# Performance work log

Measured on AMD Instinct MI355X. Metric: run time of the kernel, lower is better.

The kernel has to match this reference:

```python
import jax, jax.numpy as jnp
import numpy as np

B, L, C, H, W = 8, 8, 64, 56, 56
K = 3
EPS = 1e-5


def setup_inputs() -> dict:
    key = jax.random.key(0)
    ks = jax.random.split(key, 7)
    s = lambda k, shape, sc=0.05: jax.random.normal(k, shape, dtype=jnp.float32) * sc
    return {
        "x": jax.random.normal(ks[0], (B, L, C, H, W), dtype=jnp.float32),
        "temporal_w": s(ks[1], (C, C)),        # Conv3d 1x1x1 C->C
        "temporal_b": s(ks[2], (C,)),
        "fc_w": s(ks[3], (C,)),                # Conv3d 1x1x1 C->1
        "fc_b": s(ks[4], (1,)),
        "conv_w": s(ks[5], (C, C, K, K), 0.1), # self.weight [1,1,Co,Ci,k,k] core
        "conv_b": s(ks[6], (C,)),              # self.bias [1,1,Co] core
        "bn_gamma": jnp.ones((C,), jnp.float32),
        "bn_beta": jnp.zeros((C,), jnp.float32),
    }


def reference(x, temporal_w, temporal_b, fc_w, fc_b, conv_w, conv_b, bn_gamma, bn_beta):
    b, l, c, h, w = x.shape
    # ---- generateweight_fourier ----
    xin = jnp.transpose(x, (0, 2, 1, 3, 4))                # [B,C,L,H,W]
    f = jnp.fft.fft2(xin, axes=(3, 4), norm='ortho')       # spatial FFT
    f = jnp.fft.fft(f, axis=2, norm='ortho')               # temporal FFT
    allxin = xin + 0.01 * jnp.abs(f) * xin                 # Fourier2 attention + residual
    pooled = allxin.mean(axis=(3, 4))                      # AdaptiveAvgPool3d((None,1,1)) -> [B,C,L]
    # temporalconv: 1x1x1 Conv3d C->C on [B,C,L,1,1]
    calib = jnp.einsum('oc,bcl->bol', temporal_w, pooled) + temporal_b[None, :, None]  # [B,C,L]
    # fc: 1x1x1 Conv3d C->1
    fcout = jnp.einsum('c,bcl->bl', fc_w, pooled) + fc_b[0]                            # [B,L]
    # finalweight: weight[1,1,Co,Ci,k,k] * (calib+1) broadcast over Ci -> [B,L,Co,Ci,k,k]
    calib_blc = jnp.transpose(calib, (0, 2, 1)) + 1.0      # [B,L,Ci]
    fw = conv_w[None, None] * calib_blc[:, :, None, :, None, None]
    fb = conv_b[None, None, :] * (fcout + 1.0)[:, :, None] # [B,L,Co]
    # ---- dynamic per-(sample,frame) conv2d (groups = b*l) ----
    x_flat = x.reshape(b * l, c, h, w)
    fw_flat = fw.reshape(b * l, c, c, K, K)
    fb_flat = fb.reshape(b * l, c)

    def per_sample(xi, wi):
        return jax.lax.conv_general_dilated(
            xi[None], wi, window_strides=(1, 1), padding=[(1, 1), (1, 1)],
            dimension_numbers=('NCHW', 'OIHW', 'NCHW'))[0]

    out = jax.vmap(per_sample)(x_flat, fw_flat) + fb_flat[:, :, None, None]
    out = x_flat + out                                     # residual (gate=False)
    # BatchNorm2d (training-mode batch statistics)
    mean = out.mean(axis=(0, 2, 3), keepdims=True)
    var = out.var(axis=(0, 2, 3), keepdims=True)
    out = (out - mean) * jax.lax.rsqrt(var + EPS)
    out = out * bn_gamma[None, :, None, None] + bn_beta[None, :, None, None]
    out = out * jax.nn.sigmoid(out)                        # SiLU
    return out.reshape(b, l, c, h, w)
```

## Files before the change

### kernel.cpp

```cpp
#include <hip/hip_runtime.h>
#include <cmath>

#define HW 3136
#define NF 64
#define NBLK2 448
#define YROWS 29
#define YPX 1624

typedef __attribute__((ext_vector_type(8))) short short8;
typedef __attribute__((ext_vector_type(4))) float float4a;

__device__ __forceinline__ unsigned short f2bf(float f) {
    unsigned int u = __float_as_uint(f);
    u += 0x7fffu + ((u >> 16) & 1u);
    return (unsigned short)(u >> 16);
}
__device__ __forceinline__ float bf2f(unsigned short u) {
    return __uint_as_float(((unsigned int)u) << 16);
}

__global__ __launch_bounds__(256)
void pack_kernel(const float* __restrict__ cw,
                 unsigned short* __restrict__ Ffix,
                 unsigned short* __restrict__ Wp,
                 unsigned short* __restrict__ Fs1) {
    if (blockIdx.x < 64) {
        int idx = blockIdx.x * 256 + threadIdx.x;
        int j    = idx & 7;
        int lane = (idx >> 3) & 63;
        int ks   = (idx >> 9) & 3;
        int t    = (idx >> 11) & 3;
        int p    = (idx >> 13) & 1;
        int mn = t * 16 + (lane & 15);
        int k  = ks * 32 + (lane >> 4) * 8 + j;
        float val = 0.f;
        if (mn < 56 && k < 112) {
            int h = k >> 1;
            int prod = (mn * h) % 56;
            float ang = -6.2831853071795864f * (float)prod / 56.0f;
            float cr = cosf(ang);
            float ci = sinf(ang);
            if (p == 0) val = (k & 1) ? -ci : cr;
            else        val = (k & 1) ?  cr : ci;
        }
        Ffix[idx] = f2bf(val);
    } else if (blockIdx.x < 208) {
        int idx = (blockIdx.x - 64) * 256 + threadIdx.x;
        if (idx < 36864) {
            int i  = idx & 63;
            int o  = (idx >> 6) & 63;
            int kk = idx >> 12;
            Wp[idx] = f2bf(cw[(o * 64 + i) * 9 + kk]);
        }
    } else {
        int idx = (blockIdx.x - 208) * 256 + threadIdx.x;
        int j  = idx & 7;
        int ln = (idx >> 3) & 63;
        int ks = (idx >> 9) & 1;
        int mt = (idx >> 10) & 3;
        int m = mt * 16 + (ln & 15);
        int k = ks * 32 + (ln >> 4) * 8 + j;
        float val = 0.f;
        if (k < 56) {
            if (m < 29) {
                int prod = (m * k) % 56;
                val = cosf(-6.2831853071795864f * (float)prod / 56.0f);
            } else if (m >= 32 && m < 61) {
                int mm = m - 32;
                int prod = (mm * k) % 56;
                val = sinf(-6.2831853071795864f * (float)prod / 56.0f);
            }
        }
        Fs1[idx] = f2bf(val);
    }
}

__global__ __launch_bounds__(256)
void dft2d_kernel(const float* __restrict__ x,
                  const unsigned short* __restrict__ Fs1,
                  const unsigned short* __restrict__ Ffix,
                  unsigned short* __restrict__ Y) {
    const int bid = blockIdx.x;
    const int l  = bid & 7;
    const int bc = bid >> 3;
    const int c  = bc & 63;
    const int b  = bc >> 6;
    const int tid  = threadIdx.x;
    const int lane = tid & 63;
    const int wv   = tid >> 6;
    const int n    = lane & 15;
    const int q    = lane >> 4;

    __shared__ unsigned short xT[64 * 68];
    __shared__ unsigned short P[32 * 136];

    for (int t = tid; t < 656; t += 256) {
        if (t < 384) ((unsigned int*)xT)[(t / 6) * 34 + 28 + (t % 6)] = 0u;
        else         ((unsigned int*)xT)[56 * 34 + (t - 384)] = 0u;
    }
    const float* xp = x + ((size_t)((b * 8 + l) * 64 + c)) * HW;
    for (int t = tid; t < 784; t += 256) {
        int h = t / 14, w4 = t - h * 14;
        float4 v = *(const float4*)(xp + h * 56 + w4 * 4);
        xT[(w4 * 4 + 0) * 68 + h] = f2bf(v.x);
        xT[(w4 * 4 + 1) * 68 + h] = f2bf(v.y);
        xT[(w4 * 4 + 2) * 68 + h] = f2bf(v.z);
        xT[(w4 * 4 + 3) * 68 + h] = f2bf(v.w);
    }
    __syncthreads();

    {
        float4a acc[4];
        #pragma unroll
        for (int nt = 0; nt < 4; ++nt) acc[nt] = (float4a){0.f, 0.f, 0.f, 0.f};
        #pragma unroll
        for (int ks = 0; ks < 2; ++ks) {
            short8 afr = *(const short8*)(Fs1 + ((size_t)((wv * 2 + ks) * 64 + lane)) * 8);
            #pragma unroll
            for (int nt = 0; nt < 4; ++nt) {
                short8 bfr = *(const short8*)(xT + (nt * 16 + n) * 68 + ks * 32 + q * 8);
                acc[nt] = __builtin_amdgcn_mfma_f32_16x16x32_bf16(afr, bfr, acc[nt], 0, 0, 0);
            }
        }
        #pragma unroll
        for (int nt = 0; nt < 4; ++nt)
            #pragma unroll
            for (int r = 0; r < 4; ++r) {
                int m = wv * 16 + q * 4 + r;
                P[(m & 31) * 136 + 2 * (nt * 16 + n) + (m >> 5)] = f2bf(acc[nt][r]);
            }
    }
    __syncthreads();

    {
        const int p  = wv >> 1;
        const int ch = wv & 1;
        short8 afr[2][4];
        #pragma unroll
        for (int mt = 0; mt < 2; ++mt)
            #pragma unroll
            for (int ks = 0; ks < 4; ++ks)
                afr[mt][ks] = *(const short8*)(P + (mt * 16 + n) * 136 + ks * 32 + q * 8);
        float4a acc[2][2];
        #pragma unroll
        for (int mt = 0; mt < 2; ++mt)
            #pragma unroll
            for (int u = 0; u < 2; ++u) acc[mt][u] = (float4a){0.f, 0.f, 0.f, 0.f};
        #pragma unroll
        for (int ks = 0; ks < 4; ++ks)
            #pragma unroll
            for (int u = 0; u < 2; ++u) {
                int nt = ch * 2 + u;
                short8 bfr = *(const short8*)(Ffix + ((size_t)(((p * 4 + nt) * 4 + ks) * 64 + lane)) * 8);
                #pragma unroll
                for (int mt = 0; mt < 2; ++mt)
                    acc[mt][u] = __builtin_amdgcn_mfma_f32_16x16x32_bf16(afr[mt][ks], bfr, acc[mt][u], 0, 0, 0);
            }
        unsigned short* Yo = Y + ((size_t)bid * 2 + p) * YPX;
        #pragma unroll
        for (int mt = 0; mt < 2; ++mt)
            #pragma unroll
            for (int u = 0; u < 2; ++u)
                #pragma unroll
                for (int r = 0; r < 4; ++r) {
                    int row = mt * 16 + q * 4 + r;
                    int col = (ch * 2 + u) * 16 + n;
                    if (row < YROWS && col < 56)
                        Yo[row * 56 + col] = f2bf(acc[mt][u][r]);
                }
    }
}

__global__ __launch_bounds__(256)
void combine_kernel(const float* __restrict__ x,
                    const unsigned short* __restrict__ Y,
                    float* __restrict__ pooled) {
    const int bc = blockIdx.x;
    const int c  = bc & 63;
    const int b  = bc >> 6;
    const int tid  = threadIdx.x;
    const int lane = tid & 63;
    const int wv   = tid >> 6;

    const float SQH = 0.70710678118654752f;
    const float c8[8] = {1.f,  SQH, 0.f, -SQH, -1.f, -SQH, 0.f,  SQH};
    const float s8[8] = {0.f, -SQH, -1.f, -SQH, 0.f,  SQH, 1.f,  SQH};

    float S[8], X[8];
    #pragma unroll
    for (int i = 0; i < 8; ++i) { S[i] = 0.f; X[i] = 0.f; }

    const size_t xbase = ((size_t)(b * 8) * 64 + c) * HW;
    const unsigned short* Yb = Y + (size_t)bc * 16 * YPX;

    for (int t = tid; t < YPX; t += 256) {
        int kh = t / 56, kw = t - kh * 56;
        float Yr[8], Yi[8];
        #pragma unroll
        for (int l = 0; l < 8; ++l) {
            Yr[l] = bf2f(Yb[(l * 2 + 0) * YPX + t]);
            Yi[l] = bf2f(Yb[(l * 2 + 1) * YPX + t]);
        }
        float mag[8];
        #pragma unroll
        for (int tt = 0; tt < 8; ++tt) {
            float gr = 0.f, gi = 0.f;
            #pragma unroll
            for (int l = 0; l < 8; ++l) {
                const int k = (tt * l) & 7;
                gr += c8[k] * Yr[l] - s8[k] * Yi[l];
                gi += c8[k] * Yi[l] + s8[k] * Yr[l];
            }
            mag[tt] = sqrtf(gr * gr + gi * gi);
        }
        const bool mir = (kh >= 1 && kh <= 27);
        const int tm = (56 - kh) * 56 + (kw ? 56 - kw : 0);
        #pragma unroll
        for (int l = 0; l < 8; ++l) {
            float xb = x[xbase + (size_t)l * 64 * HW + t];
            S[l] += mag[l] * xb;
            X[l] += xb;
            if (mir) {
                float xm = x[xbase + (size_t)l * 64 * HW + tm];
                S[l] += mag[(8 - l) & 7] * xm;
                X[l] += xm;
            }
        }
    }

    __shared__ float red[4][16];
    #pragma unroll
    for (int i = 0; i < 8; ++i) {
        #pragma unroll
        for (int m = 1; m < 64; m <<= 1) {
            S[i] += __shfl_xor(S[i], m);
            X[i] += __shfl_xor(X[i], m);
        }
    }
    if (lane == 0) {
        #pragma unroll
        for (int i = 0; i < 8; ++i) { red[wv][i] = S[i]; red[wv][8 + i] = X[i]; }
    }
    __syncthreads();
    if (tid < 8) {
        float s = 0.f, xs = 0.f;
        #pragma unroll
        for (int w = 0; w < 4; ++w) { s += red[w][tid]; xs += red[w][8 + tid]; }
        const float kS = 0.01f / (56.0f * 2.8284271247461903f);
        pooled[bc * 8 + tid] = (xs + kS * s) / 3136.0f;
    }
}

__global__ __launch_bounds__(64)
void calib_kernel(const float* __restrict__ pooled,
                  const float* __restrict__ tw_, const float* __restrict__ tb,
                  const float* __restrict__ fcw, const float* __restrict__ fcb,
                  const float* __restrict__ convb,
                  float* __restrict__ scale, float* __restrict__ fbias) {
    const int nn = blockIdx.x;
    const int b = nn >> 3, l = nn & 7;
    const int o = threadIdx.x;
    const float* pr = pooled + b * 512 + l;
    float dot = 0.f;
    #pragma unroll 8
    for (int c0 = 0; c0 < 64; ++c0) dot += tw_[o * 64 + c0] * pr[c0 * 8];
    float fcp = fcw[o] * pr[o * 8];
    #pragma unroll
    for (int off = 32; off > 0; off >>= 1) fcp += __shfl_down(fcp, off);
    float fcout = __shfl(fcp, 0) + fcb[0];
    scale[nn * 64 + o] = 1.0f + tb[o] + dot;
    fbias[nn * 64 + o] = convb[o] * (fcout + 1.0f);
}

__global__ __launch_bounds__(256, 2)
void conv_mfma_kernel(const float* __restrict__ x,
                      const unsigned short* __restrict__ Wp,
                      const float* __restrict__ scale, const float* __restrict__ fbias,
                      float* __restrict__ out,
                      float* __restrict__ psum, float* __restrict__ psum2) {
    const int rt = blockIdx.x;
    const int nn = blockIdx.y;
    const int tid  = threadIdx.x;
    const int lane = tid & 63;
    const int wv   = tid >> 6;
    const int r0   = rt * 8;

    __shared__ unsigned short xs[10 * 60 * 64];
    __shared__ float fb[64], ssc[64], rsc[64], bn1[64], bn2[64];

    if (tid < 64) {
        fb[tid]  = fbias[nn * 64 + tid];
        float s  = scale[nn * 64 + tid];
        ssc[tid] = s;
        rsc[tid] = 1.0f / s;
        bn1[tid] = 0.f; bn2[tid] = 0.f;
    }
    __syncthreads();

    for (int t = tid; t < 10240; t += 256) {
        if (t < 8960) {
            int c4 = t % 14;
            int rr = (t / 14) % 10;
            int i  = t / 140;
            int gr = r0 - 1 + rr;
            float4 v = make_float4(0.f, 0.f, 0.f, 0.f);
            if (gr >= 0 && gr < 56)
                v = *(const float4*)(x + ((size_t)(nn * 64 + i) * HW + gr * 56 + c4 * 4));
            float s = ssc[i];
            int g = i >> 3, il = i & 7;
            float vv[4] = {v.x, v.y, v.z, v.w};
            #pragma unroll
            for (int j = 0; j < 4; ++j) {
                int lc = c4 * 4 + 1 + j;
                xs[(rr * 60 + lc) * 64 + (((g ^ (lc & 7)) << 3) | il)] = f2bf(vv[j] * s);
            }
        } else {
            int idx = t - 8960;
            int i   = idx / 20;
            int rem = idx - i * 20;
            int rr  = rem >> 1;
            int lc  = (rem & 1) * 57;
            int g = i >> 3, il = i & 7;
            xs[(rr * 60 + lc) * 64 + (((g ^ (lc & 7)) << 3) | il)] = 0;
        }
    }
    __syncthreads();

    const int pxo = lane & 15;
    const int q   = lane >> 4;

    float4a acc[7][4];
    #pragma unroll
    for (int j = 0; j < 7; ++j)
        #pragma unroll
        for (int ot = 0; ot < 4; ++ot) acc[j][ot] = (float4a){0.f, 0.f, 0.f, 0.f};

    int rp[7], cp[7];
    #pragma unroll
    for (int j = 0; j < 7; ++j) {
        int px = (wv * 7 + j) * 16 + pxo;
        rp[j] = px / 56;
        cp[j] = px - rp[j] * 56;
    }

    #pragma unroll 1
    for (int kk = 0; kk < 9; ++kk) {
        const int dr = kk / 3, dc = kk - dr * 3;
        short8 a[4][2];
        #pragma unroll
        for (int ot = 0; ot < 4; ++ot)
            #pragma unroll
            for (int ih = 0; ih < 2; ++ih)
                a[ot][ih] = *(const short8*)(Wp + ((kk * 64 + ot * 16 + pxo) * 64 + ih * 32 + q * 8));

        #pragma unroll
        for (int j = 0; j < 7; ++j) {
            int lc = cp[j] + dc;
            int base = ((rp[j] + dr) * 60 + lc) * 64;
            int sw = lc & 7;
            #pragma unroll
            for (int ih = 0; ih < 2; ++ih) {
                short8 bv = *(const short8*)&xs[base + (((q + ih * 4) ^ sw) << 3)];
                #pragma unroll
                for (int ot = 0; ot < 4; ++ot)
                    acc[j][ot] = __builtin_amdgcn_mfma_f32_16x16x32_bf16(a[ot][ih], bv, acc[j][ot], 0, 0, 0);
            }
        }
    }

    float bs[4][4], bs2[4][4];
    #pragma unroll
    for (int ot = 0; ot < 4; ++ot)
        #pragma unroll
        for (int r = 0; r < 4; ++r) { bs[ot][r] = 0.f; bs2[ot][r] = 0.f; }

    #pragma unroll
    for (int j = 0; j < 7; ++j) {
        int px  = (wv * 7 + j) * 16 + pxo;
        int gpx = r0 * 56 + px;
        int rr  = rp[j] + 1;
        int lc  = cp[j] + 1;
        int sw  = lc & 7;
        int rowbase = (rr * 60 + lc) * 64;
        #pragma unroll
        for (int ot = 0; ot < 4; ++ot) {
            int g  = ot * 2 + (q >> 1);
            ushort4 uu = *(const ushort4*)(xs + rowbase + (((g ^ sw) << 3) | ((q & 1) * 4)));
            float resid[4] = {bf2f(uu.x), bf2f(uu.y), bf2f(uu.z), bf2f(uu.w)};
            #pragma unroll
            for (int r = 0; r < 4; ++r) {
                int o = ot * 16 + q * 4 + r;
                size_t off = (size_t)(nn * 64 + o) * HW + gpx;
                float v = acc[j][ot][r] + resid[r] * rsc[o] + fb[o];
                out[off] = v;
                bs[ot][r]  += v;
                bs2[ot][r] += v * v;
            }
        }
    }
    #pragma unroll
    for (int ot = 0; ot < 4; ++ot)
        #pragma unroll
        for (int r = 0; r < 4; ++r) {
            #pragma unroll
            for (int m = 1; m < 16; m <<= 1) {
                bs[ot][r]  += __shfl_xor(bs[ot][r], m);
                bs2[ot][r] += __shfl_xor(bs2[ot][r], m);
            }
        }
    if (pxo == 0) {
        #pragma unroll
        for (int ot = 0; ot < 4; ++ot)
            #pragma unroll
            for (int r = 0; r < 4; ++r) {
                int o = ot * 16 + q * 4 + r;
                atomicAdd(&bn1[o], bs[ot][r]);
                atomicAdd(&bn2[o], bs2[ot][r]);
            }
    }
    __syncthreads();
    if (tid < 64) {
        int bl = nn * 7 + rt;
        psum[bl * 64 + tid]  = bn1[tid];
        psum2[bl * 64 + tid] = bn2[tid];
    }
}

__global__ __launch_bounds__(256)
void bnstat_kernel(const float* __restrict__ psum, const float* __restrict__ psum2,
                   float* __restrict__ bn) {
    const int o = blockIdx.x;
    const int tid = threadIdx.x;
    float s = 0.f, s2 = 0.f;
    for (int bl = tid; bl < NBLK2; bl += 256) {
        s  += psum[bl * 64 + o];
        s2 += psum2[bl * 64 + o];
    }
    __shared__ float r1[256], r2[256];
    r1[tid] = s; r2[tid] = s2;
    __syncthreads();
    for (int st = 128; st > 0; st >>= 1) {
        if (tid < st) { r1[tid] += r1[tid + st]; r2[tid] += r2[tid + st]; }
        __syncthreads();
    }
    if (tid == 0) {
        const float N = 64.0f * (float)HW;
        float mean = r1[0] / N;
        float var  = r2[0] / N - mean * mean;
        bn[o]      = mean;
        bn[64 + o] = rsqrtf(var + 1e-5f);
    }
}

__global__ __launch_bounds__(256)
void bnsilu_kernel(float* __restrict__ out, const float* __restrict__ bn,
                   const float* __restrict__ gamma, const float* __restrict__ beta) {
    size_t idx = (size_t)blockIdx.x * 256 + threadIdx.x;
    if (idx >= (size_t)NF * 64 * HW) return;
    int c = (int)((idx / HW) & 63);
    float v = out[idx];
    float y = (v - bn[c]) * bn[64 + c] * gamma[c] + beta[c];
    out[idx] = y / (1.0f + expf(-y));
}

extern "C" void kernel_launch(void* const* d_in, const int* in_sizes, int n_in,
                              void* d_out, int out_size, void* d_ws, size_t ws_size,
                              hipStream_t stream) {
    const float* x          = (const float*)d_in[0];
    const float* temporal_w = (const float*)d_in[1];
    const float* temporal_b = (const float*)d_in[2];
    const float* fc_w       = (const float*)d_in[3];
    const float* fc_b       = (const float*)d_in[4];
    const float* conv_w     = (const float*)d_in[5];
    const float* conv_b     = (const float*)d_in[6];
    const float* bn_gamma   = (const float*)d_in[7];
    const float* bn_beta    = (const float*)d_in[8];
    float* out = (float*)d_out;
    float* ws  = (float*)d_ws;

    float* pooled = ws;
    float* scale  = ws + 4096;
    float* fbias  = ws + 8192;
    unsigned short* Wp = (unsigned short*)(ws + 12288);
    float* psum   = ws + 12288 + 18432;
    float* psum2  = psum + NBLK2 * 64;
    float* bn     = psum2 + NBLK2 * 64;
    unsigned short* Ffix = (unsigned short*)(bn + 128);
    unsigned short* Fs1  = Ffix + 16384;

    unsigned short* Y = (unsigned short*)out;

    pack_kernel<<<224, 256, 0, stream>>>(conv_w, Ffix, Wp, Fs1);
    dft2d_kernel<<<4096, 256, 0, stream>>>(x, Fs1, Ffix, Y);
    combine_kernel<<<512, 256, 0, stream>>>(x, Y, pooled);
    calib_kernel<<<64, 64, 0, stream>>>(pooled, temporal_w, temporal_b,
                                        fc_w, fc_b, conv_b, scale, fbias);
    conv_mfma_kernel<<<dim3(7, 64), 256, 0, stream>>>(x, Wp, scale, fbias,
                                                      out, psum, psum2);
    bnstat_kernel<<<64, 256, 0, stream>>>(psum, psum2, bn);
    int total = NF * 64 * HW;
    bnsilu_kernel<<<(total + 255) / 256, 256, 0, stream>>>(out, bn, bn_gamma, bn_beta);
}
```

Measured before the change: 235.6 us.

## Halve conv row tile, rehash LDS swizzle, stage combine magnitudes in shared memory

The conv kernel now handles 4 output rows per block instead of 8. That doubles the grid to 14x64 blocks and shrinks the LDS tile and accumulator registers, so more blocks can be resident per CU, at the cost of reloading more halo rows. The LDS swizzle key changes from lc&7 to an XOR hash of lc, intended to reduce bank conflicts for the shifted-column reads. In combine_kernel, the FFT magnitudes are first written to a shared buffer and x is then read once in a linear pass with a symmetry lookup, replacing the strided mirrored reads of x.

```diff
diff --git a/kernel.cpp b/kernel.cpp
--- a/kernel.cpp
+++ b/kernel.cpp
@@ -3,7 +3,7 @@
 
 #define HW 3136
 #define NF 64
-#define NBLK2 448
+#define NBLK2 896
 #define YROWS 29
 #define YPX 1624
 
@@ -17,6 +17,9 @@
 }
 __device__ __forceinline__ float bf2f(unsigned short u) {
     return __uint_as_float(((unsigned int)u) << 16);
+}
+__device__ __forceinline__ int lchash(int lc) {
+    return (lc ^ (lc >> 2)) & 7;
 }
 
 __global__ __launch_bounds__(256)
@@ -182,26 +185,22 @@
     const int lane = tid & 63;
     const int wv   = tid >> 6;
 
+    __shared__ float mg[8 * YPX];
+    __shared__ float red[4][16];
+
     const float SQH = 0.70710678118654752f;
     const float c8[8] = {1.f,  SQH, 0.f, -SQH, -1.f, -SQH, 0.f,  SQH};
     const float s8[8] = {0.f, -SQH, -1.f, -SQH, 0.f,  SQH, 1.f,  SQH};
 
-    float S[8], X[8];
-    #pragma unroll
-    for (int i = 0; i < 8; ++i) { S[i] = 0.f; X[i] = 0.f; }
-
-    const size_t xbase = ((size_t)(b * 8) * 64 + c) * HW;
     const unsigned short* Yb = Y + (size_t)bc * 16 * YPX;
 
     for (int t = tid; t < YPX; t += 256) {
-        int kh = t / 56, kw = t - kh * 56;
         float Yr[8], Yi[8];
         #pragma unroll
         for (int l = 0; l < 8; ++l) {
             Yr[l] = bf2f(Yb[(l * 2 + 0) * YPX + t]);
             Yi[l] = bf2f(Yb[(l * 2 + 1) * YPX + t]);
         }
-        float mag[8];
         #pragma unroll
         for (int tt = 0; tt < 8; ++tt) {
             float gr = 0.f, gi = 0.f;
@@ -211,24 +210,29 @@
                 gr += c8[k] * Yr[l] - s8[k] * Yi[l];
                 gi += c8[k] * Yi[l] + s8[k] * Yr[l];
             }
-            mag[tt] = sqrtf(gr * gr + gi * gi);
-        }
-        const bool mir = (kh >= 1 && kh <= 27);
-        const int tm = (56 - kh) * 56 + (kw ? 56 - kw : 0);
+            mg[tt * YPX + t] = sqrtf(gr * gr + gi * gi);
+        }
+    }
+    __syncthreads();
+
+    float S[8], X[8];
+    #pragma unroll
+    for (int i = 0; i < 8; ++i) { S[i] = 0.f; X[i] = 0.f; }
+    const size_t xbase = ((size_t)(b * 8) * 64 + c) * HW;
+
+    for (int t = tid; t < 3136; t += 256) {
+        int kh = t / 56, kw = t - kh * 56;
+        bool flip = (kh > 28);
+        int bt = flip ? ((56 - kh) * 56 + (kw ? 56 - kw : 0)) : t;
         #pragma unroll
         for (int l = 0; l < 8; ++l) {
-            float xb = x[xbase + (size_t)l * 64 * HW + t];
-            S[l] += mag[l] * xb;
-            X[l] += xb;
-            if (mir) {
-                float xm = x[xbase + (size_t)l * 64 * HW + tm];
-                S[l] += mag[(8 - l) & 7] * xm;
-                X[l] += xm;
-            }
-        }
-    }
-
-    __shared__ float red[4][16];
+            float xv = x[xbase + (size_t)l * 64 * HW + t];
+            int sel = flip ? ((8 - l) & 7) : l;
+            S[l] += mg[sel * YPX + bt] * xv;
+            X[l] += xv;
+        }
+    }
+
     #pragma unroll
     for (int i = 0; i < 8; ++i) {
         #pragma unroll
@@ -283,9 +287,9 @@
     const int tid  = threadIdx.x;
     const int lane = tid & 63;
     const int wv   = tid >> 6;
-    const int r0   = rt * 8;
-
-    __shared__ unsigned short xs[10 * 60 * 64];
+    const int r0   = rt * 4;
+
+    __shared__ unsigned short xs[6 * 60 * 64];
     __shared__ float fb[64], ssc[64], rsc[64], bn1[64], bn2[64];
 
     if (tid < 64) {
@@ -297,11 +301,11 @@
     }
     __syncthreads();
 
-    for (int t = tid; t < 10240; t += 256) {
-        if (t < 8960) {
+    for (int t = tid; t < 6144; t += 256) {
+        if (t < 5376) {
             int c4 = t % 14;
-            int rr = (t / 14) % 10;
-            int i  = t / 140;
+            int rr = (t / 14) % 6;
+            int i  = t / 84;
             int gr = r0 - 1 + rr;
             float4 v = make_float4(0.f, 0.f, 0.f, 0.f);
             if (gr >= 0 && gr < 56)
@@ -312,33 +316,36 @@
             #pragma unroll
             for (int j = 0; j < 4; ++j) {
                 int lc = c4 * 4 + 1 + j;
-                xs[(rr * 60 + lc) * 64 + (((g ^ (lc & 7)) << 3) | il)] = f2bf(vv[j] * s);
+                xs[(rr * 60 + lc) * 64 + (((g ^ lchash(lc)) << 3) | il)] = f2bf(vv[j] * s);
             }
         } else {
-            int idx = t - 8960;
-            int i   = idx / 20;
-            int rem = idx - i * 20;
+            int idx = t - 5376;
+            int i   = idx / 12;
+            int rem = idx - i * 12;
             int rr  = rem >> 1;
             int lc  = (rem & 1) * 57;
             int g = i >> 3, il = i & 7;
-            xs[(rr * 60 + lc) * 64 + (((g ^ (lc & 7)) << 3) | il)] = 0;
+            xs[(rr * 60 + lc) * 64 + (((g ^ lchash(lc)) << 3) | il)] = 0;
         }
     }
     __syncthreads();
 
     const int pxo = lane & 15;
     const int q   = lane >> 4;
-
-    float4a acc[7][4];
-    #pragma unroll
-    for (int j = 0; j < 7; ++j)
+    const int tb  = (wv * 7) >> 1;
+    const int cnt = (((wv + 1) * 7) >> 1) - tb;
+
+    float4a acc[4][4];
+    #pragma unroll
+    for (int j = 0; j < 4; ++j)
         #pragma unroll
         for (int ot = 0; ot < 4; ++ot) acc[j][ot] = (float4a){0.f, 0.f, 0.f, 0.f};
 
-    int rp[7], cp[7];
-    #pragma unroll
-    for (int j = 0; j < 7; ++j) {
-        int px = (wv * 7 + j) * 16 + pxo;
+    int rp[4], cp[4];
+    #pragma unroll
+    for (int j = 0; j < 4; ++j) {
+        int tile = tb + ((j < cnt) ? j : 0);
+        int px = tile * 16 + pxo;
         rp[j] = px / 56;
         cp[j] = px - rp[j] * 56;
     }
@@ -354,10 +361,10 @@
                 a[ot][ih] = *(const short8*)(Wp + ((kk * 64 + ot * 16 + pxo) * 64 + ih * 32 + q * 8));
 
         #pragma unroll
-        for (int j = 0; j < 7; ++j) {
+        for (int j = 0; j < 4; ++j) {
             int lc = cp[j] + dc;
             int base = ((rp[j] + dr) * 60 + lc) * 64;
-            int sw = lc & 7;
+            int sw = lchash(lc);
             #pragma unroll
             for (int ih = 0; ih < 2; ++ih) {
                 short8 bv = *(const short8*)&xs[base + (((q + ih * 4) ^ sw) << 3)];
@@ -375,26 +382,28 @@
         for (int r = 0; r < 4; ++r) { bs[ot][r] = 0.f; bs2[ot][r] = 0.f; }
 
     #pragma unroll
-    for (int j = 0; j < 7; ++j) {
-        int px  = (wv * 7 + j) * 16 + pxo;
-        int gpx = r0 * 56 + px;
-        int rr  = rp[j] + 1;
-        int lc  = cp[j] + 1;
-        int sw  = lc & 7;
-        int rowbase = (rr * 60 + lc) * 64;
-        #pragma unroll
-        for (int ot = 0; ot < 4; ++ot) {
-            int g  = ot * 2 + (q >> 1);
-            ushort4 uu = *(const ushort4*)(xs + rowbase + (((g ^ sw) << 3) | ((q & 1) * 4)));
-            float resid[4] = {bf2f(uu.x), bf2f(uu.y), bf2f(uu.z), bf2f(uu.w)};
-            #pragma unroll
-            for (int r = 0; r < 4; ++r) {
-                int o = ot * 16 + q * 4 + r;
-                size_t off = (size_t)(nn * 64 + o) * HW + gpx;
-                float v = acc[j][ot][r] + resid[r] * rsc[o] + fb[o];
-                out[off] = v;
-                bs[ot][r]  += v;
-                bs2[ot][r] += v * v;
+    for (int j = 0; j < 4; ++j) {
+        if (j < cnt) {
+            int px  = (tb + j) * 16 + pxo;
+            int gpx = r0 * 56 + px;
+            int rr  = rp[j] + 1;
+            int lc  = cp[j] + 1;
+            int sw  = lchash(lc);
+            int rowbase = (rr * 60 + lc) * 64;
+            #pragma unroll
+            for (int ot = 0; ot < 4; ++ot) {
+                int g  = ot * 2 + (q >> 1);
+                ushort4 uu = *(const ushort4*)(xs + rowbase + (((g ^ sw) << 3) | ((q & 1) * 4)));
+                float resid[4] = {bf2f(uu.x), bf2f(uu.y), bf2f(uu.z), bf2f(uu.w)};
+                #pragma unroll
+                for (int r = 0; r < 4; ++r) {
+                    int o = ot * 16 + q * 4 + r;
+                    size_t off = (size_t)(nn * 64 + o) * HW + gpx;
+                    float v = acc[j][ot][r] + resid[r] * rsc[o] + fb[o];
+                    out[off] = v;
+                    bs[ot][r]  += v;
+                    bs2[ot][r] += v * v;
+                }
             }
         }
     }
@@ -420,7 +429,7 @@
     }
     __syncthreads();
     if (tid < 64) {
-        int bl = nn * 7 + rt;
+        int bl = nn * 14 + rt;
         psum[bl * 64 + tid]  = bn1[tid];
         psum2[bl * 64 + tid] = bn2[tid];
     }
@@ -495,8 +504,8 @@
     combine_kernel<<<512, 256, 0, stream>>>(x, Y, pooled);
     calib_kernel<<<64, 64, 0, stream>>>(pooled, temporal_w, temporal_b,
                                         fc_w, fc_b, conv_b, scale, fbias);
-    conv_mfma_kernel<<<dim3(7, 64), 256, 0, stream>>>(x, Wp, scale, fbias,
-                                                      out, psum, psum2);
+    conv_mfma_kernel<<<dim3(14, 64), 256, 0, stream>>>(x, Wp, scale, fbias,
+                                                       out, psum, psum2);
     bnstat_kernel<<<64, 256, 0, stream>>>(psum, psum2, bn);
     int total = NF * 64 * HW;
     bnsilu_kernel<<<(total + 255) / 256, 256, 0, stream>>>(out, bn, bn_gamma, bn_beta);
```

Measured after the change: 236.5 us. No clear change (+0.4%).
